# Kernel tuning notes

Measured on AMD Instinct MI355X. Metric: run time of the kernel, lower is better.

## Reference

```python
import jax, jax.numpy as jnp
import numpy as np

N = 50000   # nodes
E = 800000  # edges (avg degree 16)
H = 128     # hidden_channels
G = 50      # num_gaussians
CUT = 6.0   # cutoff
PI = float(np.pi)
SHIFT = float(np.log(2.0))


def ssp(x):
    # ShiftedSoftplus
    return jax.nn.softplus(x) - SHIFT


def setup_inputs() -> dict:
    key = jax.random.key(0)
    ks = jax.random.split(key, 32)
    p = lambda k, shape: jax.random.normal(k, shape, jnp.float32) * 0.05
    inp = {
        "z": jax.random.normal(ks[0], (N, 3), jnp.float32),
        "dist": jax.random.uniform(ks[1], (E,), jnp.float32) * CUT,
        "edge_index": jax.random.randint(ks[2], (2, E), 0, N, dtype=jnp.int32),
        "init_w": p(ks[3], (3, H)), "init_b": jnp.zeros((H,), jnp.float32),
        # layer 0
        "e0_lin_w": p(ks[4], (H, H)),
        "e0_m0_w": p(ks[5], (G, H)), "e0_m0_b": jnp.zeros((H,), jnp.float32),
        "e0_m2_w": p(ks[6], (H, H)), "e0_m2_b": jnp.zeros((H,), jnp.float32),
        "v0_l1_w": p(ks[7], (H, H)), "v0_l1_b": jnp.zeros((H,), jnp.float32),
        "v0_l2_w": p(ks[8], (H, H)), "v0_l2_b": jnp.zeros((H,), jnp.float32),
        # layer 1
        "e1_lin_w": p(ks[9], (H, H)),
        "e1_m0_w": p(ks[10], (G, H)), "e1_m0_b": jnp.zeros((H,), jnp.float32),
        "e1_m2_w": p(ks[11], (H, H)), "e1_m2_b": jnp.zeros((H,), jnp.float32),
        "v1_l1_w": p(ks[12], (H, H)), "v1_l1_b": jnp.zeros((H,), jnp.float32),
        "v1_l2_w": p(ks[13], (H, H)), "v1_l2_b": jnp.zeros((H,), jnp.float32),
        # readout
        "u_l1_w": p(ks[14], (H, H)), "u_l1_b": jnp.zeros((H,), jnp.float32),
        "u_l2_w": p(ks[15], (H, 3)), "u_l2_b": jnp.zeros((3,), jnp.float32),
    }
    return inp


def reference(z, dist, edge_index, init_w, init_b,
              e0_lin_w, e0_m0_w, e0_m0_b, e0_m2_w, e0_m2_b,
              v0_l1_w, v0_l1_b, v0_l2_w, v0_l2_b,
              e1_lin_w, e1_m0_w, e1_m0_b, e1_m2_w, e1_m2_b,
              v1_l1_w, v1_l1_b, v1_l2_w, v1_l2_b,
              u_l1_w, u_l1_b, u_l2_w, u_l2_b):
    n = z.shape[0]
    j, i = edge_index[0], edge_index[1]  # source, target

    # RBF embedding of dist.to(long)  (torch truncates toward zero)
    offset = jnp.linspace(0.0, CUT, G, dtype=jnp.float32)
    coeff = -0.5 / (offset[1] - offset[0]) ** 2
    demb = jnp.exp(coeff * (jnp.trunc(dist)[:, None] - offset[None, :]) ** 2)  # [E,G]

    # cosine cutoff gate
    C = 0.5 * (jnp.cos(dist * (PI / CUT)) + 1.0)  # [E]

    v = z @ init_w + init_b  # [N,H]

    layers = [
        (e0_lin_w, e0_m0_w, e0_m0_b, e0_m2_w, e0_m2_b, v0_l1_w, v0_l1_b, v0_l2_w, v0_l2_b),
        (e1_lin_w, e1_m0_w, e1_m0_b, e1_m2_w, e1_m2_b, v1_l1_w, v1_l1_b, v1_l2_w, v1_l2_b),
    ]
    for lin_w, m0_w, m0_b, m2_w, m2_b, l1_w, l1_b, l2_w, l2_b in layers:
        # update_e: filter MLP on RBF, gated by cutoff, times gathered node feats
        W = (ssp(demb @ m0_w + m0_b) @ m2_w + m2_b) * C[:, None]  # [E,H]
        e = (v @ lin_w)[j] * W                                     # [E,H]
        # update_v: scatter-add into target nodes, then node MLP + residual
        agg = jax.ops.segment_sum(e, i, num_segments=n)            # [N,H]
        v = v + (ssp(agg @ l1_w + l1_b) @ l2_w + l2_b)

    # update_u readout
    return ssp(v @ u_l1_w + u_l1_b) @ u_l2_w + u_l2_b  # [N,3]
```

## Files before the change

### kernel.cpp

```cpp
#include <hip/hip_runtime.h>
#include <cstdint>
#include <cstddef>

#define HD 128
#define GD 50
static constexpr float PI_F   = 3.14159265358979323846f;
static constexpr float CUTF   = 6.0f;
static constexpr float SHIFTF = 0.69314718055994530942f;

typedef _Float16 f16x8 __attribute__((ext_vector_type(8)));
typedef _Float16 f16x2 __attribute__((ext_vector_type(2)));
typedef float    f32x4 __attribute__((ext_vector_type(4)));

struct Ptr8 { const float* p[8]; };

__device__ __forceinline__ float ssp(float x) {
    float e = __expf(-fabsf(x));
    return fmaxf(x, 0.0f) + __logf(1.0f + e) - SHIFTF;
}

__device__ __forceinline__ _Float16* t16(_Float16* base, int row, int byte) {
    return (_Float16*)((char*)base + row * 256 + (byte ^ ((row & 7) << 4)));
}

__device__ __forceinline__ void mfma_ct(const f16x8 af[4],
                                        const _Float16* __restrict__ Bf,
                                        int lane, f32x4 acc[2], int ctb) {
    #pragma unroll
    for (int ks = 0; ks < 4; ++ks)
        #pragma unroll
        for (int c = 0; c < 2; ++c)
            acc[c] = __builtin_amdgcn_mfma_f32_16x16x32_f16(
                af[ks], ((const f16x8*)Bf)[((ctb + c) * 4 + ks) * 64 + lane],
                acc[c], 0, 0, 0);
}

template <int ACT>
__device__ __forceinline__ void acc_to_t16_ct(const f32x4 acc[2], const float* bias,
                                              int lane, _Float16* tile, int ctb) {
    int col0 = lane & 15, r0 = (lane >> 4) * 4;
    #pragma unroll
    for (int c = 0; c < 2; ++c) {
        int cc = (ctb + c) * 16 + col0;
        float bs = bias ? bias[cc] : 0.f;
        #pragma unroll
        for (int r = 0; r < 4; ++r) {
            float o = acc[c][r] + bs;
            if (ACT) o = ssp(o);
            *t16(tile, r0 + r, cc * 2) = (_Float16)o;
        }
    }
}

__device__ __forceinline__ void t16_to_af(_Float16* tile, int lane, f16x8 af[4]) {
    int row = lane & 15, kgB = (lane >> 4) * 16;
    #pragma unroll
    for (int ks = 0; ks < 4; ++ks)
        af[ks] = *(const f16x8*)t16(tile, row, ks * 64 + kgB);
}

__device__ __forceinline__ void vz_ct(const float* __restrict__ z,
                                      const float* __restrict__ iw,
                                      const float* __restrict__ ib,
                                      int rowbase, int lane, int n, int ctb,
                                      f32x4 vz[2]) {
    int col0 = lane & 15, r0 = (lane >> 4) * 4;
    float zr[4][3];
    #pragma unroll
    for (int r = 0; r < 4; ++r) {
        int row = min(rowbase + r0 + r, n - 1);
        zr[r][0] = z[row * 3 + 0];
        zr[r][1] = z[row * 3 + 1];
        zr[r][2] = z[row * 3 + 2];
    }
    #pragma unroll
    for (int c = 0; c < 2; ++c) {
        int cc = (ctb + c) * 16 + col0;
        float w0 = iw[cc], w1 = iw[HD + cc], w2 = iw[2 * HD + cc], bz = ib[cc];
        #pragma unroll
        for (int r = 0; r < 4; ++r)
            vz[c][r] = fmaf(zr[r][0], w0, fmaf(zr[r][1], w1, fmaf(zr[r][2], w2, bz)));
    }
}

__global__ __launch_bounds__(HD) void k_wtab2(Ptr8 P, float* __restrict__ wtab) {
    const int bin = blockIdx.x, layer = blockIdx.y;
    const int t = threadIdx.x;
    const float* m0w = P.p[layer * 4 + 0];
    const float* m0b = P.p[layer * 4 + 1];
    const float* m2w = P.p[layer * 4 + 2];
    const float* m2b = P.p[layer * 4 + 3];
    __shared__ float hbuf[HD];

    const float spacing = CUTF / (GD - 1);
    const float coeff   = -0.5f / (spacing * spacing);

    float acc = m0b[t];
    #pragma unroll 5
    for (int g = 0; g < GD; ++g) {
        float d = (float)bin - (float)g * spacing;
        acc = fmaf(__expf(coeff * d * d), m0w[g * HD + t], acc);
    }
    hbuf[t] = ssp(acc);
    __syncthreads();

    float acc2 = m2b[t];
    #pragma unroll 8
    for (int k = 0; k < HD; ++k)
        acc2 = fmaf(hbuf[k], m2w[k * HD + t], acc2);
    wtab[(layer * 7 + bin) * HD + t] = acc2;
}

__global__ __launch_bounds__(256) void k_prepB7(Ptr8 P, _Float16* __restrict__ Bf,
                                                int* __restrict__ deg, int n) {
    int slot = blockIdx.y;
    int idx = blockIdx.x * 256 + threadIdx.x;
    if (slot == 7) {
        for (int i = idx; i < n; i += 2048) deg[i] = 0;
        return;
    }
    if (idx >= 2048) return;
    const float* W = P.p[slot];
    int l  = idx & 63;
    int f  = idx >> 6;
    int ks = f & 3, ct = f >> 2;
    int col = ct * 16 + (l & 15);
    int k0  = ks * 32 + ((l >> 4) << 3);
    f16x8 o;
    #pragma unroll
    for (int j = 0; j < 8; ++j) o[j] = (_Float16)W[(size_t)(k0 + j) * HD + col];
    ((f16x8*)(Bf + (size_t)slot * 16384))[idx] = o;
}

__global__ __launch_bounds__(256) void k_deg(const int* __restrict__ ei,
                                             int* __restrict__ deg, int nedges) {
    int e = blockIdx.x * 256 + threadIdx.x;
    if (e < nedges) atomicAdd(&deg[ei[nedges + e]], 1);
}

__global__ __launch_bounds__(1024) void k_scan1(const int* __restrict__ deg,
                                                int* __restrict__ rowstart,
                                                int* __restrict__ blocksum, int n) {
    __shared__ int wsum[16];
    int tid  = threadIdx.x;
    int lane = tid & 63, wid = tid >> 6;
    int i = blockIdx.x * 1024 + tid;
    int val = (i < n) ? deg[i] : 0;
    int x = val;
    #pragma unroll
    for (int off = 1; off < 64; off <<= 1) {
        int y = __shfl_up(x, off, 64);
        if (lane >= off) x += y;
    }
    if (lane == 63) wsum[wid] = x;
    __syncthreads();
    if (wid == 0) {
        int s = (lane < 16) ? wsum[lane] : 0;
        #pragma unroll
        for (int off = 1; off < 16; off <<= 1) {
            int y = __shfl_up(s, off, 64);
            if (lane >= off) s += y;
        }
        if (lane < 16) wsum[lane] = s;
    }
    __syncthreads();
    int wbase = (wid > 0) ? wsum[wid - 1] : 0;
    if (i <= n) rowstart[i] = wbase + x - val;
    if (tid == 1023) blocksum[blockIdx.x] = wsum[15];
}

__global__ __launch_bounds__(64) void k_scan2(int* __restrict__ blocksum, int nb) {
    int lane = threadIdx.x;
    int v = (lane < nb) ? blocksum[lane] : 0;
    int x = v;
    #pragma unroll
    for (int off = 1; off < 64; off <<= 1) {
        int y = __shfl_up(x, off, 64);
        if (lane >= off) x += y;
    }
    if (lane < nb) blocksum[lane] = x - v;
}

__global__ __launch_bounds__(1024) void k_scan3(int* __restrict__ rowstart,
                                                int* __restrict__ cursor,
                                                const int* __restrict__ blocksum,
                                                int n) {
    int i = blockIdx.x * 1024 + threadIdx.x;
    if (i <= n) {
        int rs = rowstart[i] + blocksum[blockIdx.x];
        rowstart[i] = rs;
        if (i < n) cursor[i] = rs;
    }
}

__global__ __launch_bounds__(256) void k_epos(const int* __restrict__ ei,
                                              int* __restrict__ cursor,
                                              int* __restrict__ pos,
                                              int nedges) {
    int base = blockIdx.x * 2048 + threadIdx.x;
    int p[8];
    #pragma unroll
    for (int k = 0; k < 8; ++k) {
        int e = base + k * 256;
        if (e < nedges) p[k] = atomicAdd(&cursor[ei[nedges + e]], 1);
    }
    #pragma unroll
    for (int k = 0; k < 8; ++k) {
        int e = base + k * 256;
        if (e < nedges) pos[e] = p[k];
    }
}

__global__ __launch_bounds__(256) void k_ewrite(const int* __restrict__ ei,
                                                const float* __restrict__ dist,
                                                const int* __restrict__ pos,
                                                int2* __restrict__ ecomb,
                                                int nedges) {
    int base = blockIdx.x * 2048 + threadIdx.x;
    #pragma unroll
    for (int k = 0; k < 8; ++k) {
        int e = base + k * 256;
        if (e < nedges) {
            int   j = ei[e];
            float d = dist[e];
            int bin = min((int)d, 6);
            float Cg = 0.5f * (cosf(d * (PI_F / CUTF)) + 1.0f);
            ecomb[pos[e]] = make_int2(j | (bin << 25), __float_as_int(Cg));
        }
    }
}

__global__ __launch_bounds__(256) void k_front(const float* __restrict__ z,
                                               const float* __restrict__ iw,
                                               const float* __restrict__ ib,
                                               const _Float16* __restrict__ BfL,
                                               _Float16* __restrict__ vlin_h, int n) {
    __shared__ __attribute__((aligned(16))) _Float16 tile16[2048];
    int tid = threadIdx.x, lane = tid & 63, wid = tid >> 6;
    int rowbase = blockIdx.x * 16;
    int arow = min(rowbase + (lane & 15), n - 1);
    float z0 = z[arow * 3 + 0], z1 = z[arow * 3 + 1], z2 = z[arow * 3 + 2];
    int kg = (lane >> 4) * 8;

    f16x8 af[4];
    #pragma unroll
    for (int ks = 0; ks < 4; ++ks) {
        f16x8 h;
        #pragma unroll
        for (int j = 0; j < 8; ++j) {
            int c = ks * 32 + kg + j;
            h[j] = (_Float16)fmaf(z0, iw[c], fmaf(z1, iw[HD + c], fmaf(z2, iw[2 * HD + c], ib[c])));
        }
        af[ks] = h;
    }

    f32x4 acc[2];
    acc[0] = (f32x4){0.f, 0.f, 0.f, 0.f};
    acc[1] = (f32x4){0.f, 0.f, 0.f, 0.f};
    mfma_ct(af, BfL, lane, acc, wid * 2);
    acc_to_t16_ct<0>(acc, nullptr, lane, tile16, wid * 2);
    __syncthreads();
    int row = tid >> 4, g8 = tid & 15;
    if (rowbase + row < n)
        ((f16x8*)vlin_h)[(size_t)(rowbase + row) * 16 + g8] =
            *(const f16x8*)t16(tile16, row, g8 * 16);
}

__global__ __launch_bounds__(256) void k_agg(const int* __restrict__ rowstart,
                                             const int2* __restrict__ ecomb,
                                             const _Float16* __restrict__ vlin_h,
                                             const float* __restrict__ wtab,
                                             _Float16* __restrict__ agg_h, int n) {
    __shared__ float lwt[7 * HD];
    int tid = threadIdx.x;
    if (tid < 224) ((float4*)lwt)[tid] = ((const float4*)wtab)[tid];
    __syncthreads();

    int node = blockIdx.x * 4 + (tid >> 6);
    if (node >= n) return;
    int lane = tid & 63;
    int beg = rowstart[node], end = rowstart[node + 1];

    float accx = 0.f, accy = 0.f;
    const float* lwt2 = lwt + 2 * lane;
    int e = beg;
    for (; e + 7 < end; e += 8) {
        int2 cc[8];
        #pragma unroll
        for (int k = 0; k < 8; ++k) cc[k] = ecomb[e + k];
        f16x2 hh[8];
        #pragma unroll
        for (int k = 0; k < 8; ++k)
            hh[k] = *(const f16x2*)(vlin_h + (size_t)(cc[k].x & 0x01FFFFFF) * HD + 2 * lane);
        float2 ww[8];
        #pragma unroll
        for (int k = 0; k < 8; ++k)
            ww[k] = *(const float2*)(lwt2 + (cc[k].x >> 25) * HD);
        #pragma unroll
        for (int k = 0; k < 8; ++k) {
            float g = __int_as_float(cc[k].y);
            accx = fmaf((float)hh[k][0], ww[k].x * g, accx);
            accy = fmaf((float)hh[k][1], ww[k].y * g, accy);
        }
    }
    for (; e + 3 < end; e += 4) {
        int2 cc[4];
        #pragma unroll
        for (int k = 0; k < 4; ++k) cc[k] = ecomb[e + k];
        #pragma unroll
        for (int k = 0; k < 4; ++k) {
            f16x2 h = *(const f16x2*)(vlin_h + (size_t)(cc[k].x & 0x01FFFFFF) * HD + 2 * lane);
            float2 w = *(const float2*)(lwt2 + (cc[k].x >> 25) * HD);
            float g = __int_as_float(cc[k].y);
            accx = fmaf((float)h[0], w.x * g, accx);
            accy = fmaf((float)h[1], w.y * g, accy);
        }
    }
    for (; e < end; ++e) {
        int2 c0 = ecomb[e];
        f16x2 h0 = *(const f16x2*)(vlin_h + (size_t)(c0.x & 0x01FFFFFF) * HD + 2 * lane);
        float2 w0 = *(const float2*)(lwt2 + (c0.x >> 25) * HD);
        float g0 = __int_as_float(c0.y);
        accx = fmaf((float)h0[0], w0.x * g0, accx);
        accy = fmaf((float)h0[1], w0.y * g0, accy);
    }
    f16x2 o; o[0] = (_Float16)accx; o[1] = (_Float16)accy;
    *(f16x2*)(agg_h + (size_t)node * HD + 2 * lane) = o;
}

__global__ __launch_bounds__(256) void k_mid(const _Float16* __restrict__ agg_h,
                                             const _Float16* __restrict__ Bf1,
                                             const float* __restrict__ b1,
                                             const _Float16* __restrict__ Bf2,
                                             const float* __restrict__ b2,
                                             const _Float16* __restrict__ BfL,
                                             const float* __restrict__ z,
                                             const float* __restrict__ iw,
                                             const float* __restrict__ ib,
                                             f32x4* __restrict__ vres4,
                                             _Float16* __restrict__ vlin_h, int n) {
    __shared__ __attribute__((aligned(16))) _Float16 tile16[2048];
    int tid = threadIdx.x, lane = tid & 63, wid = tid >> 6;
    int rowbase = blockIdx.x * 16;
    int ctb = wid * 2;

    int arow = min(rowbase + (lane & 15), n - 1);
    int kg = (lane >> 4) * 8;
    f16x8 af[4];
    #pragma unroll
    for (int ks = 0; ks < 4; ++ks)
        af[ks] = *(const f16x8*)(agg_h + (size_t)arow * HD + ks * 32 + kg);

    f32x4 acc[2];
    acc[0] = (f32x4){0.f, 0.f, 0.f, 0.f};
    acc[1] = (f32x4){0.f, 0.f, 0.f, 0.f};
    mfma_ct(af, Bf1, lane, acc, ctb);
    acc_to_t16_ct<1>(acc, b1, lane, tile16, ctb);
    __syncthreads();
    t16_to_af(tile16, lane, af);
    __syncthreads();

    acc[0] = (f32x4){0.f, 0.f, 0.f, 0.f};
    acc[1] = (f32x4){0.f, 0.f, 0.f, 0.f};
    mfma_ct(af, Bf2, lane, acc, ctb);

    f32x4 vz[2];
    vz_ct(z, iw, ib, rowbase, lane, n, ctb, vz);
    int col0 = lane & 15;
    #pragma unroll
    for (int c = 0; c < 2; ++c) {
        float bs = b2[(ctb + c) * 16 + col0];
        #pragma unroll
        for (int r = 0; r < 4; ++r) acc[c][r] += bs + vz[c][r];
        vres4[((size_t)blockIdx.x * 8 + ctb + c) * 64 + lane] = acc[c];
    }

    acc_to_t16_ct<0>(acc, nullptr, lane, tile16, ctb);
    __syncthreads();
    t16_to_af(tile16, lane, af);
    __syncthreads();

    acc[0] = (f32x4){0.f, 0.f, 0.f, 0.f};
    acc[1] = (f32x4){0.f, 0.f, 0.f, 0.f};
    mfma_ct(af, BfL, lane, acc, ctb);
    acc_to_t16_ct<0>(acc, nullptr, lane, tile16, ctb);
    __syncthreads();
    int row = tid >> 4, g8 = tid & 15;
    if (rowbase + row < n)
        ((f16x8*)vlin_h)[(size_t)(rowbase + row) * 16 + g8] =
            *(const f16x8*)t16(tile16, row, g8 * 16);
}

__global__ __launch_bounds__(256) void k_back(const _Float16* __restrict__ agg_h,
                                              const _Float16* __restrict__ Bf1,
                                              const float* __restrict__ b1,
                                              const _Float16* __restrict__ Bf2,
                                              const float* __restrict__ b2,
                                              const _Float16* __restrict__ BfU,
                                              const float* __restrict__ ub1,
                                              const float* __restrict__ w2,
                                              const float* __restrict__ ub2,
                                              const f32x4* __restrict__ vres4,
                                              float* __restrict__ out, int n) {
    __shared__ __attribute__((aligned(16))) _Float16 tile16[2048];
    __shared__ float red[4][16][3];
    int tid = threadIdx.x, lane = tid & 63, wid = tid >> 6;
    int rowbase = blockIdx.x * 16;
    int ctb = wid * 2;

    int arow = min(rowbase + (lane & 15), n - 1);
    int kg = (lane >> 4) * 8;
    f16x8 af[4];
    #pragma unroll
    for (int ks = 0; ks < 4; ++ks)
        af[ks] = *(const f16x8*)(agg_h + (size_t)arow * HD + ks * 32 + kg);

    f32x4 acc[2];
    acc[0] = (f32x4){0.f, 0.f, 0.f, 0.f};
    acc[1] = (f32x4){0.f, 0.f, 0.f, 0.f};
    mfma_ct(af, Bf1, lane, acc, ctb);
    acc_to_t16_ct<1>(acc, b1, lane, tile16, ctb);
    __syncthreads();
    t16_to_af(tile16, lane, af);
    __syncthreads();

    acc[0] = (f32x4){0.f, 0.f, 0.f, 0.f};
    acc[1] = (f32x4){0.f, 0.f, 0.f, 0.f};
    mfma_ct(af, Bf2, lane, acc, ctb);

    int col0 = lane & 15;
    #pragma unroll
    for (int c = 0; c < 2; ++c) {
        float bs = b2[(ctb + c) * 16 + col0];
        f32x4 rv = vres4[((size_t)blockIdx.x * 8 + ctb + c) * 64 + lane];
        #pragma unroll
        for (int r = 0; r < 4; ++r) acc[c][r] += bs + rv[r];
    }

    acc_to_t16_ct<0>(acc, nullptr, lane, tile16, ctb);
    __syncthreads();
    t16_to_af(tile16, lane, af);

    acc[0] = (f32x4){0.f, 0.f, 0.f, 0.f};
    acc[1] = (f32x4){0.f, 0.f, 0.f, 0.f};
    mfma_ct(af, BfU, lane, acc, ctb);

    int r0 = (lane >> 4) * 4;
    float p0[4] = {0.f, 0.f, 0.f, 0.f};
    float p1[4] = {0.f, 0.f, 0.f, 0.f};
    float p2[4] = {0.f, 0.f, 0.f, 0.f};
    #pragma unroll
    for (int c = 0; c < 2; ++c) {
        int cc = (ctb + c) * 16 + col0;
        float bu = ub1[cc];
        float w20 = w2[cc * 3 + 0], w21 = w2[cc * 3 + 1], w22 = w2[cc * 3 + 2];
        #pragma unroll
        for (int r = 0; r < 4; ++r) {
            float u = ssp(acc[c][r] + bu);
            p0[r] = fmaf(u, w20, p0[r]);
            p1[r] = fmaf(u, w21, p1[r]);
            p2[r] = fmaf(u, w22, p2[r]);
        }
    }
    #pragma unroll
    for (int m = 1; m < 16; m <<= 1) {
        #pragma unroll
        for (int r = 0; r < 4; ++r) {
            p0[r] += __shfl_xor(p0[r], m, 64);
            p1[r] += __shfl_xor(p1[r], m, 64);
            p2[r] += __shfl_xor(p2[r], m, 64);
        }
    }
    if (col0 == 0) {
        #pragma unroll
        for (int r = 0; r < 4; ++r) {
            red[wid][r0 + r][0] = p0[r];
            red[wid][r0 + r][1] = p1[r];
            red[wid][r0 + r][2] = p2[r];
        }
    }
    __syncthreads();
    if (tid < 48) {
        int row = tid / 3, c = tid % 3;
        float s = red[0][row][c] + red[1][row][c] + red[2][row][c] + red[3][row][c];
        if (rowbase + row < n)
            out[(size_t)(rowbase + row) * 3 + c] = s + ub2[c];
    }
}

extern "C" void kernel_launch(void* const* d_in, const int* in_sizes, int n_in,
                              void* d_out, int out_size, void* d_ws, size_t ws_size,
                              hipStream_t stream) {
    const float* z      = (const float*)d_in[0];
    const float* dist   = (const float*)d_in[1];
    const int*   ei     = (const int*)d_in[2];
    const float* init_w = (const float*)d_in[3];
    const float* init_b = (const float*)d_in[4];

    const float* L[2][9];
    for (int l = 0; l < 2; ++l)
        for (int p = 0; p < 9; ++p)
            L[l][p] = (const float*)d_in[5 + l * 9 + p];

    const float* u_l1_w = (const float*)d_in[23];
    const float* u_l1_b = (const float*)d_in[24];
    const float* u_l2_w = (const float*)d_in[25];
    const float* u_l2_b = (const float*)d_in[26];
    float* out = (float*)d_out;

    const int N = in_sizes[0] / 3;
    const int E = in_sizes[1];

    const int nb16     = (N + 15) / 16;
    const int e8Grid   = (E + 2047) / 2048;
    const int edgeGrid = (E + 255) / 256;
    const int scanB    = (N + 1 + 1023) / 1024;
    const int aggGrid  = (N + 3) / 4;

    float* wtab   = (float*)d_ws;
    float* bf     = wtab + 2048;
    float* vres   = bf + 57344;
    float* vh     = vres + (size_t)nb16 * 2048;
    float* aggh   = vh + (size_t)N * 64;
    int2*  ecomb  = (int2*)(aggh + (size_t)N * 64);
    int*   pos    = (int*)(ecomb + E);
    int*   deg    = pos + E;
    int*   rowstart = deg + N;
    int*   cursor = rowstart + N + 1;
    int*   blocksum = cursor + N;

    _Float16* vlin_h = (_Float16*)vh;
    _Float16* agg_h  = (_Float16*)aggh;
    f32x4*    vres4  = (f32x4*)vres;
    _Float16* Bf     = (_Float16*)bf;
    _Float16* BfW[7];
    for (int i = 0; i < 7; ++i) BfW[i] = Bf + (size_t)i * 16384;

    Ptr8 wt; wt.p[0] = L[0][1]; wt.p[1] = L[0][2]; wt.p[2] = L[0][3]; wt.p[3] = L[0][4];
             wt.p[4] = L[1][1]; wt.p[5] = L[1][2]; wt.p[6] = L[1][3]; wt.p[7] = L[1][4];
    k_wtab2<<<dim3(7, 2), HD, 0, stream>>>(wt, wtab);

    Ptr8 pb; pb.p[0] = L[0][0]; pb.p[1] = L[0][5]; pb.p[2] = L[0][7];
             pb.p[3] = L[1][0]; pb.p[4] = L[1][5]; pb.p[5] = L[1][7];
             pb.p[6] = u_l1_w;  pb.p[7] = u_l1_w;
    k_prepB7<<<dim3(8, 8), 256, 0, stream>>>(pb, Bf, deg, N);

    k_deg<<<edgeGrid, 256, 0, stream>>>(ei, deg, E);
    k_scan1<<<scanB, 1024, 0, stream>>>(deg, rowstart, blocksum, N);
    k_scan2<<<1, 64, 0, stream>>>(blocksum, scanB);
    k_scan3<<<scanB, 1024, 0, stream>>>(rowstart, cursor, blocksum, N);
    k_epos<<<e8Grid, 256, 0, stream>>>(ei, cursor, pos, E);
    k_ewrite<<<e8Grid, 256, 0, stream>>>(ei, dist, pos, ecomb, E);

    k_front<<<nb16, 256, 0, stream>>>(z, init_w, init_b, BfW[0], vlin_h, N);
    k_agg<<<aggGrid, 256, 0, stream>>>(rowstart, ecomb, vlin_h, wtab, agg_h, N);
    k_mid<<<nb16, 256, 0, stream>>>(agg_h, BfW[1], L[0][6], BfW[2], L[0][8],
                                    BfW[3], z, init_w, init_b, vres4, vlin_h, N);
    k_agg<<<aggGrid, 256, 0, stream>>>(rowstart, ecomb, vlin_h, wtab + 7 * HD, agg_h, N);
    k_back<<<nb16, 256, 0, stream>>>(agg_h, BfW[4], L[1][6], BfW[5], L[1][8],
                                     BfW[6], u_l1_b, u_l2_w, u_l2_b, vres4, out, N);
}
```

Baseline: 350.3 us.

## Merge CSR build kernels: derive edge slots from degree atomics, fold scan passes

The degree-count atomic now also returns each edge's local slot within its target row, so the separate cursor pass and its second round of atomics go away. The final slot is rowstart plus that local offset. The two small scan-fixup kernels are merged into one that recomputes the block-sum prefix in every block, and the weight-table and weight-prep kernels are merged into a single launch. This cuts the number of kernel launches and one pass of atomics over the edges, at the cost of an extra rowstart gather per edge in the write kernel.

Measured after the change: 316.1 us. 9.8% less time.

```diff
diff --git a/kernel.cpp b/kernel.cpp
--- a/kernel.cpp
+++ b/kernel.cpp
@@ -83,14 +83,40 @@
     }
 }
 
-__global__ __launch_bounds__(HD) void k_wtab2(Ptr8 P, float* __restrict__ wtab) {
-    const int bin = blockIdx.x, layer = blockIdx.y;
-    const int t = threadIdx.x;
-    const float* m0w = P.p[layer * 4 + 0];
-    const float* m0b = P.p[layer * 4 + 1];
-    const float* m2w = P.p[layer * 4 + 2];
-    const float* m2b = P.p[layer * 4 + 3];
-    __shared__ float hbuf[HD];
+__global__ __launch_bounds__(256) void k_wtab_prep(Ptr8 WT, Ptr8 PB,
+                                                   float* __restrict__ wtab,
+                                                   _Float16* __restrict__ Bf,
+                                                   int* __restrict__ deg, int n) {
+    int y = blockIdx.y;
+    if (y < 7) {
+        int idx = blockIdx.x * 256 + threadIdx.x;
+        if (idx >= 2048) return;
+        const float* W = PB.p[y];
+        int l  = idx & 63;
+        int f  = idx >> 6;
+        int ks = f & 3, ct = f >> 2;
+        int col = ct * 16 + (l & 15);
+        int k0  = ks * 32 + ((l >> 4) << 3);
+        f16x8 o;
+        #pragma unroll
+        for (int j = 0; j < 8; ++j) o[j] = (_Float16)W[(size_t)(k0 + j) * HD + col];
+        ((f16x8*)(Bf + (size_t)y * 16384))[idx] = o;
+        return;
+    }
+    if (y == 7) {
+        int idx = blockIdx.x * 256 + threadIdx.x;
+        for (int i = idx; i < n; i += 2048) deg[i] = 0;
+        return;
+    }
+    if (blockIdx.x >= 7) return;
+    int bin   = blockIdx.x;
+    int layer = threadIdx.x >> 7;
+    int t     = threadIdx.x & 127;
+    const float* m0w = WT.p[layer * 4 + 0];
+    const float* m0b = WT.p[layer * 4 + 1];
+    const float* m2w = WT.p[layer * 4 + 2];
+    const float* m2b = WT.p[layer * 4 + 3];
+    __shared__ float hbuf[2][HD];
 
     const float spacing = CUTF / (GD - 1);
     const float coeff   = -0.5f / (spacing * spacing);
@@ -101,41 +127,32 @@
         float d = (float)bin - (float)g * spacing;
         acc = fmaf(__expf(coeff * d * d), m0w[g * HD + t], acc);
     }
-    hbuf[t] = ssp(acc);
+    hbuf[layer][t] = ssp(acc);
     __syncthreads();
 
     float acc2 = m2b[t];
     #pragma unroll 8
     for (int k = 0; k < HD; ++k)
-        acc2 = fmaf(hbuf[k], m2w[k * HD + t], acc2);
+        acc2 = fmaf(hbuf[layer][k], m2w[k * HD + t], acc2);
     wtab[(layer * 7 + bin) * HD + t] = acc2;
 }
 
-__global__ __launch_bounds__(256) void k_prepB7(Ptr8 P, _Float16* __restrict__ Bf,
-                                                int* __restrict__ deg, int n) {
-    int slot = blockIdx.y;
-    int idx = blockIdx.x * 256 + threadIdx.x;
-    if (slot == 7) {
-        for (int i = idx; i < n; i += 2048) deg[i] = 0;
-        return;
-    }
-    if (idx >= 2048) return;
-    const float* W = P.p[slot];
-    int l  = idx & 63;
-    int f  = idx >> 6;
-    int ks = f & 3, ct = f >> 2;
-    int col = ct * 16 + (l & 15);
-    int k0  = ks * 32 + ((l >> 4) << 3);
-    f16x8 o;
-    #pragma unroll
-    for (int j = 0; j < 8; ++j) o[j] = (_Float16)W[(size_t)(k0 + j) * HD + col];
-    ((f16x8*)(Bf + (size_t)slot * 16384))[idx] = o;
-}
-
-__global__ __launch_bounds__(256) void k_deg(const int* __restrict__ ei,
-                                             int* __restrict__ deg, int nedges) {
-    int e = blockIdx.x * 256 + threadIdx.x;
-    if (e < nedges) atomicAdd(&deg[ei[nedges + e]], 1);
+__global__ __launch_bounds__(256) void k_degpos(const int* __restrict__ ei,
+                                                int* __restrict__ deg,
+                                                int* __restrict__ pos,
+                                                int nedges) {
+    int base = blockIdx.x * 2048 + threadIdx.x;
+    int p[8];
+    #pragma unroll
+    for (int k = 0; k < 8; ++k) {
+        int e = base + k * 256;
+        if (e < nedges) p[k] = atomicAdd(&deg[ei[nedges + e]], 1);
+    }
+    #pragma unroll
+    for (int k = 0; k < 8; ++k) {
+        int e = base + k * 256;
+        if (e < nedges) pos[e] = p[k];
+    }
 }
 
 __global__ __launch_bounds__(1024) void k_scan1(const int* __restrict__ deg,
@@ -169,51 +186,32 @@
     if (tid == 1023) blocksum[blockIdx.x] = wsum[15];
 }
 
-__global__ __launch_bounds__(64) void k_scan2(int* __restrict__ blocksum, int nb) {
-    int lane = threadIdx.x;
-    int v = (lane < nb) ? blocksum[lane] : 0;
-    int x = v;
-    #pragma unroll
-    for (int off = 1; off < 64; off <<= 1) {
-        int y = __shfl_up(x, off, 64);
-        if (lane >= off) x += y;
-    }
-    if (lane < nb) blocksum[lane] = x - v;
-}
-
-__global__ __launch_bounds__(1024) void k_scan3(int* __restrict__ rowstart,
-                                                int* __restrict__ cursor,
-                                                const int* __restrict__ blocksum,
-                                                int n) {
-    int i = blockIdx.x * 1024 + threadIdx.x;
-    if (i <= n) {
-        int rs = rowstart[i] + blocksum[blockIdx.x];
-        rowstart[i] = rs;
-        if (i < n) cursor[i] = rs;
-    }
-}
-
-__global__ __launch_bounds__(256) void k_epos(const int* __restrict__ ei,
-                                              int* __restrict__ cursor,
-                                              int* __restrict__ pos,
-                                              int nedges) {
-    int base = blockIdx.x * 2048 + threadIdx.x;
-    int p[8];
-    #pragma unroll
-    for (int k = 0; k < 8; ++k) {
-        int e = base + k * 256;
-        if (e < nedges) p[k] = atomicAdd(&cursor[ei[nedges + e]], 1);
-    }
-    #pragma unroll
-    for (int k = 0; k < 8; ++k) {
-        int e = base + k * 256;
-        if (e < nedges) pos[e] = p[k];
-    }
+__global__ __launch_bounds__(1024) void k_scan3e(int* __restrict__ rowstart,
+                                                 const int* __restrict__ blocksum,
+                                                 int nb, int n) {
+    __shared__ int sbase[64];
+    int tid = threadIdx.x;
+    if (tid < 64) {
+        int v = (tid < nb) ? blocksum[tid] : 0;
+        int x = v;
+        #pragma unroll
+        for (int off = 1; off < 64; off <<= 1) {
+            int y = __shfl_up(x, off, 64);
+            if (tid >= off) x += y;
+        }
+        sbase[tid] = x;
+    }
+    __syncthreads();
+    int bx = blockIdx.x;
+    int base = (bx > 0) ? sbase[bx - 1] : 0;
+    int i = bx * 1024 + tid;
+    if (i <= n) rowstart[i] += base;
 }
 
 __global__ __launch_bounds__(256) void k_ewrite(const int* __restrict__ ei,
                                                 const float* __restrict__ dist,
                                                 const int* __restrict__ pos,
+                                                const int* __restrict__ rowstart,
                                                 int2* __restrict__ ecomb,
                                                 int nedges) {
     int base = blockIdx.x * 2048 + threadIdx.x;
@@ -221,11 +219,12 @@
     for (int k = 0; k < 8; ++k) {
         int e = base + k * 256;
         if (e < nedges) {
+            int   i = ei[nedges + e];
             int   j = ei[e];
             float d = dist[e];
             int bin = min((int)d, 6);
             float Cg = 0.5f * (cosf(d * (PI_F / CUTF)) + 1.0f);
-            ecomb[pos[e]] = make_int2(j | (bin << 25), __float_as_int(Cg));
+            ecomb[rowstart[i] + pos[e]] = make_int2(j | (bin << 25), __float_as_int(Cg));
         }
     }
 }
@@ -513,7 +512,6 @@
 
     const int nb16     = (N + 15) / 16;
     const int e8Grid   = (E + 2047) / 2048;
-    const int edgeGrid = (E + 255) / 256;
     const int scanB    = (N + 1 + 1023) / 1024;
     const int aggGrid  = (N + 3) / 4;
 
@@ -526,8 +524,7 @@
     int*   pos    = (int*)(ecomb + E);
     int*   deg    = pos + E;
     int*   rowstart = deg + N;
-    int*   cursor = rowstart + N + 1;
-    int*   blocksum = cursor + N;
+    int*   blocksum = rowstart + N + 1;
 
     _Float16* vlin_h = (_Float16*)vh;
     _Float16* agg_h  = (_Float16*)aggh;
@@ -538,19 +535,16 @@
 
     Ptr8 wt; wt.p[0] = L[0][1]; wt.p[1] = L[0][2]; wt.p[2] = L[0][3]; wt.p[3] = L[0][4];
              wt.p[4] = L[1][1]; wt.p[5] = L[1][2]; wt.p[6] = L[1][3]; wt.p[7] = L[1][4];
-    k_wtab2<<<dim3(7, 2), HD, 0, stream>>>(wt, wtab);
-
     Ptr8 pb; pb.p[0] = L[0][0]; pb.p[1] = L[0][5]; pb.p[2] = L[0][7];
              pb.p[3] = L[1][0]; pb.p[4] = L[1][5]; pb.p[5] = L[1][7];
              pb.p[6] = u_l1_w;  pb.p[7] = u_l1_w;
-    k_prepB7<<<dim3(8, 8), 256, 0, stream>>>(pb, Bf, deg, N);
-
-    k_deg<<<edgeGrid, 256, 0, stream>>>(ei, deg, E);
+
+    k_wtab_prep<<<dim3(8, 9), 256, 0, stream>>>(wt, pb, wtab, Bf, deg, N);
+
+    k_degpos<<<e8Grid, 256, 0, stream>>>(ei, deg, pos, E);
     k_scan1<<<scanB, 1024, 0, stream>>>(deg, rowstart, blocksum, N);
-    k_scan2<<<1, 64, 0, stream>>>(blocksum, scanB);
-    k_scan3<<<scanB, 1024, 0, stream>>>(rowstart, cursor, blocksum, N);
-    k_epos<<<e8Grid, 256, 0, stream>>>(ei, cursor, pos, E);
-    k_ewrite<<<e8Grid, 256, 0, stream>>>(ei, dist, pos, ecomb, E);
+    k_scan3e<<<scanB, 1024, 0, stream>>>(rowstart, blocksum, scanB, N);
+    k_ewrite<<<e8Grid, 256, 0, stream>>>(ei, dist, pos, rowstart, ecomb, E);
 
     k_front<<<nb16, 256, 0, stream>>>(z, init_w, init_b, BfW[0], vlin_h, N);
     k_agg<<<aggGrid, 256, 0, stream>>>(rowstart, ecomb, vlin_h, wtab, agg_h, N);
```
